# Kernel tuning notes

Hardware: AMD Instinct MI355X
Metric: run time of the kernel (lower is better)

## Reference

```python
import jax, jax.numpy as jnp
import numpy as np

B, N, H, DQK, DV = 2, 2048, 16, 128, 128
E = H * DV
CHUNK = 64


def setup_inputs() -> dict:
    key = jax.random.key(0)
    ks = jax.random.split(key, 11)
    w = lambda k: jax.random.normal(k, (E, E), jnp.float32) * 0.02
    return {
        "x": jax.random.normal(ks[0], (B, N, E), jnp.float32),
        "prev_state": jnp.zeros((B, H, DQK, DV), jnp.float32),
        "Wq": w(ks[1]), "bq": jnp.zeros((E,), jnp.float32),
        "Wk": w(ks[2]), "bk": jnp.zeros((E,), jnp.float32),
        "Wv": w(ks[3]), "bv": jnp.zeros((E,), jnp.float32),
        "Wg": w(ks[4]), "bg": jnp.zeros((E,), jnp.float32),
        "Wo": w(ks[5]), "bo": jnp.zeros((E,), jnp.float32),
        "start_idx": 0,
    }


def _mul_i(t):
    # multiply interleaved complex pairs by i: (a, b) -> (-b, a)
    t2 = t.reshape(*t.shape[:-1], -1, 2)
    return jnp.stack((-t2[..., 1], t2[..., 0]), axis=-1).reshape(t.shape)


def reference(x, prev_state, Wq, bq, Wk, bk, Wv, bv, Wg, bg, Wo, bo, start_idx):
    b, n, e = x.shape
    h, dqk, dv, c = H, DQK, DV, CHUNK
    q = (x @ Wq.T + bq).reshape(b, n, h, dqk)
    k = (x @ Wk.T + bk).reshape(b, n, h, dqk)
    v = (x @ Wv.T + bv).reshape(b, n, h, dv)

    # xPos-style theta shift (rotary on interleaved pairs), applied along the sequence dim
    lin = jnp.linspace(0.0, 1.0, dqk // 2)
    thetas = jnp.repeat(1.0 / (10000.0 ** lin), 2).astype(x.dtype)  # (dqk,)
    idx = (start_idx + jnp.arange(n)).astype(x.dtype)
    ang = idx[:, None] * thetas[None, :]  # (n, dqk)
    sin = jnp.sin(ang)[None, :, None, :]
    cos = jnp.cos(ang)[None, :, None, :]
    q = q * cos + _mul_i(q) * sin
    k = k * cos + _mul_i(k) * sin
    k = k / jnp.sqrt(jnp.asarray(dqk, x.dtype))

    # per-head decays: 1 - 2^(-5 - h)
    gamma = 1.0 - jnp.exp2(-5.0 - jnp.arange(h, dtype=x.dtype))  # (h,)
    i = jnp.arange(c, dtype=x.dtype)
    mask = i[:, None] >= i[None, :]
    Dmat = jnp.where(mask, gamma[:, None, None] ** jnp.where(mask, i[:, None] - i[None, :], 0.0), 0.0)  # (h,c,c)
    cross_decay = gamma[:, None] ** (i[None, :] + 1.0)   # (h,c)
    kv_decay = gamma[:, None] ** (c - 1.0 - i[None, :])  # (h,c)
    chunk_decay = gamma ** c                              # (h,)

    nc = n // c
    qc = q.reshape(b, nc, c, h, dqk).transpose(1, 0, 3, 2, 4)  # (nc,b,h,c,dqk)
    kc = k.reshape(b, nc, c, h, dqk).transpose(1, 0, 3, 2, 4)
    vc = v.reshape(b, nc, c, h, dv).transpose(1, 0, 3, 2, 4)

    def step(S, qkv):
        qi, ki, vi = qkv  # (b,h,c,d)
        att = jnp.einsum('bhid,bhjd->bhij', qi, ki) * Dmat[None]
        o = jnp.einsum('bhij,bhje->bhie', att, vi)
        o = o + jnp.einsum('bhid,bhde->bhie', qi, S) * cross_decay[None, :, :, None]
        S_new = S * chunk_decay[None, :, None, None] + jnp.einsum('bhjd,bhje->bhde', ki * kv_decay[None, :, :, None], vi)
        return S_new, o

    state, outs = jax.lax.scan(step, prev_state, (qc, kc, vc))
    ret = outs.transpose(1, 0, 3, 2, 4).reshape(b, n, h, dv)

    # GroupNorm(num_groups=h, affine=False): normalize each head over dv
    mu = ret.mean(-1, keepdims=True)
    var = ((ret - mu) ** 2).mean(-1, keepdims=True)
    ret = ((ret - mu) / jnp.sqrt(var + 1e-6)).reshape(b, n, e)

    gate = jax.nn.silu(x @ Wg.T + bg)
    out = (ret * gate) @ Wo.T + bo
    return out, state
```

## Files before the change

### kernel.cpp

```cpp
#include <hip/hip_runtime.h>
#include <hip/hip_bf16.h>
#include <stdint.h>

#define B_   2
#define N_   2048
#define H_   16
#define DQK_ 128
#define DV_  128
#define E_   2048
#define CH_  64
#define NC_  32
#define M_   (B_*N_)
#define QKVG_LD 8192

using bf16x8 = __attribute__((ext_vector_type(8))) __bf16;
using f32x4  = __attribute__((ext_vector_type(4))) float;
typedef __hip_bfloat16 bf16_t;

#define ROT_C 0.21091607f
#define KS_   0.08838834764831843f

__device__ __forceinline__ void gload_lds16(const void* g, void* l) {
  __builtin_amdgcn_global_load_lds(
      (const __attribute__((address_space(1))) void*)(uintptr_t)g,
      (__attribute__((address_space(3))) void*)(uint32_t)(uintptr_t)l,
      16, 0, 0);
}

__device__ __forceinline__ float head_log2g(int h) {
  return (float)(log2(1.0 - exp2((double)(-5 - h))));
}

__device__ __forceinline__ float bfu2f(unsigned short u) {
  unsigned int t = (unsigned int)u << 16; float f;
  __builtin_memcpy(&f, &t, 4); return f;
}
__device__ __forceinline__ unsigned short f2bfu(float f) {
  bf16_t b = __float2bfloat16(f);
  unsigned short u; __builtin_memcpy(&u, &b, 2); return u;
}

__device__ __forceinline__ void rot8(const bf16x8& v, float pos, int jp0,
                                     float scale, float* out) {
#pragma unroll
  for (int p = 0; p < 4; p++) {
    float theta = exp2f(-ROT_C * (float)(jp0 + p));
    float ang = pos * theta, s, c;
    sincosf(ang, &s, &c);
    float a = (float)v[2*p], b = (float)v[2*p+1];
    out[2*p]   = (a*c - b*s) * scale;
    out[2*p+1] = (b*c + a*s) * scale;
  }
}

__global__ __launch_bounds__(256)
void cvt_all_kernel(const float* __restrict__ x,
                    const float* __restrict__ Wq, const float* __restrict__ Wk,
                    const float* __restrict__ Wv, const float* __restrict__ Wg,
                    const float* __restrict__ Wo,
                    const float* __restrict__ bq, const float* __restrict__ bk,
                    const float* __restrict__ bv, const float* __restrict__ bg,
                    bf16_t* __restrict__ xb, bf16_t* __restrict__ wcat,
                    bf16_t* __restrict__ wob, float* __restrict__ bcat) {
  const int NX = 2097152, NW = 1048576;
  int g = blockIdx.x * 256 + threadIdx.x;
  const float* s; bf16_t* d; int si, di;
  if (g < NX) { s = x; si = g; d = xb; di = g; }
  else if (g < NX + 4*NW) {
    int t = g - NX; int r = t / NW; si = t - r*NW;
    s = (r==0) ? Wq : (r==1) ? Wk : (r==2) ? Wv : Wg; d = wcat; di = t;
  } else if (g < NX + 5*NW) {
    si = g - NX - 4*NW; s = Wo; d = wob; di = si;
  } else {
    int j = g - (NX + 5*NW);
    int which = j >> 9, i = j & 511;
    const float* bs = (which==0) ? bq : (which==1) ? bk : (which==2) ? bv : bg;
    ((float4*)bcat)[which*512 + i] = ((const float4*)bs)[i];
    return;
  }
  float4 v = ((const float4*)s)[si];
  ushort4 p;
  p.x = f2bfu(v.x); p.y = f2bfu(v.y); p.z = f2bfu(v.z); p.w = f2bfu(v.w);
  ((ushort4*)d)[di] = p;
}

template<bool OUT_BF16, int NSUB>
__global__ __launch_bounds__(512, 2)
void gemm8_kernel(const bf16_t* __restrict__ A, const bf16_t* __restrict__ Bw,
                  const float* __restrict__ bias, void* __restrict__ Cout,
                  int K, int ldc, int tilesN) {
  extern __shared__ char smem[];
  const int nwg = gridDim.x;
  const int bid = blockIdx.x;
  const int cpx = nwg >> 3;
  const int swz = (bid & 7) * cpx + (bid >> 3);
  const int tn = swz % tilesN, tm = swz / tilesN;
  const int rowT0 = tm * 256, colT0 = tn * (64 * NSUB);
  const int tid = threadIdx.x, wave = tid >> 6, lane = tid & 63;
  const int wr = wave >> 2, wc = wave & 3;
  const int l16 = lane & 15, lhi = lane >> 4;
  const int NKT = K >> 6;

  const int sw = ((tid & 7) * 16) ^ (((tid >> 3) & 7) << 4);
  const size_t aOff = (size_t)(rowT0 + (tid >> 3)) * K + (sw >> 1);
  const size_t bOff = (size_t)(colT0 + (tid >> 3)) * K + (sw >> 1);
  const uint32_t wl = wave * 1024;

  auto stage = [&](int h) {
    const int ktp = h >> 2, r = h & 3, buf = ktp & 1;
    const int k0 = ktp << 6;
    if (r < 2) {
      const uint32_t base = 65536u + buf * (8192u*NSUB) + r * (4096u*NSUB) + wl;
#pragma unroll
      for (int L = 0; L < NSUB/2; L++)
        gload_lds16(Bw + bOff + (size_t)(r * (NSUB*32) + L * 64) * K + k0,
                    smem + base + L * 8192);
    } else {
      const int half = r - 2;
      const uint32_t base = buf * 32768u + half * 16384u + wl;
#pragma unroll
      for (int L = 0; L < 2; L++)
        gload_lds16(A + aOff + (size_t)(half * 128 + L * 64) * K + k0,
                    smem + base + L * 8192);
    }
  };

  for (int h = 0; h < 6; h++) stage(h);
  if constexpr (NSUB == 4) asm volatile("s_waitcnt vmcnt(4)" ::: "memory");
  else                     asm volatile("s_waitcnt vmcnt(2)" ::: "memory");
  __builtin_amdgcn_s_barrier();
  asm volatile("" ::: "memory");
  __builtin_amdgcn_sched_barrier(0);

  f32x4 acc[8][NSUB] = {};
  bf16x8 bfr[NSUB][2], bnx[2][2];

#pragma unroll
  for (int n = 0; n < 2; n++) {
    const int r = wc * (16*NSUB) + n * 16 + l16;
#pragma unroll
    for (int ks = 0; ks < 2; ks++) {
      const int cb = ks * 64 + lhi * 16;
      bnx[n][ks] = *(const bf16x8*)(smem + 65536u + r * 128 + (cb ^ ((r & 7) << 4)));
    }
  }

  for (int kt = 0; kt < NKT; kt++) {
    const int cur = kt & 1;
    const uint32_t aB = cur * 32768u;
    const uint32_t bB = 65536u + cur * (8192u*NSUB);
#pragma unroll
    for (int p = 0; p < 4; p++) {
      if (p == 0) {
#pragma unroll
        for (int n = 0; n < 2; n++)
#pragma unroll
          for (int ks = 0; ks < 2; ks++) bfr[n][ks] = bnx[n][ks];
        if constexpr (NSUB == 4) {
#pragma unroll
          for (int n = 2; n < 4; n++) {
            const int r = wc * (16*NSUB) + n * 16 + l16;
#pragma unroll
            for (int ks = 0; ks < 2; ks++) {
              const int cb = ks * 64 + lhi * 16;
              bfr[n][ks] = *(const bf16x8*)(smem + bB + r * 128 + (cb ^ ((r & 7) << 4)));
            }
          }
        }
      }
      bf16x8 afr[2][2];
#pragma unroll
      for (int mm = 0; mm < 2; mm++) {
        const int r = wr * 128 + p * 32 + mm * 16 + l16;
#pragma unroll
        for (int ks = 0; ks < 2; ks++) {
          const int cb = ks * 64 + lhi * 16;
          afr[mm][ks] = *(const bf16x8*)(smem + aB + r * 128 + (cb ^ ((r & 7) << 4)));
        }
      }
      const int h = 4 * kt + p + 6;
      if (h < 4 * NKT) stage(h);
      __builtin_amdgcn_s_barrier();
      asm volatile("s_waitcnt lgkmcnt(0)" ::: "memory");
      __builtin_amdgcn_sched_barrier(0);
      __builtin_amdgcn_s_setprio(1);
#pragma unroll
      for (int mm = 0; mm < 2; mm++)
#pragma unroll
        for (int n = 0; n < NSUB; n++)
#pragma unroll
          for (int ks = 0; ks < 2; ks++)
            acc[2 * p + mm][n] = __builtin_amdgcn_mfma_f32_16x16x32_bf16(
                afr[mm][ks], bfr[n][ks], acc[2 * p + mm][n], 0, 0, 0);
      __builtin_amdgcn_s_setprio(0);
      if (p == 2) {
        if constexpr (NSUB == 4) asm volatile("s_waitcnt vmcnt(6)" ::: "memory");
        else                     asm volatile("s_waitcnt vmcnt(5)" ::: "memory");
      }
      if (p == 3) {
        if (kt < NKT - 2) {
          if constexpr (NSUB == 4) asm volatile("s_waitcnt vmcnt(4)" ::: "memory");
          else                     asm volatile("s_waitcnt vmcnt(2)" ::: "memory");
        } else if (kt == NKT - 2) {
          asm volatile("s_waitcnt vmcnt(0)" ::: "memory");
        }
        if (kt + 1 < NKT) {
          const uint32_t bN = 65536u + ((kt + 1) & 1) * (8192u*NSUB);
#pragma unroll
          for (int n = 0; n < 2; n++) {
            const int r = wc * (16*NSUB) + n * 16 + l16;
#pragma unroll
            for (int ks = 0; ks < 2; ks++) {
              const int cb = ks * 64 + lhi * 16;
              bnx[n][ks] = *(const bf16x8*)(smem + bN + r * 128 + (cb ^ ((r & 7) << 4)));
            }
          }
        }
      }
      __builtin_amdgcn_s_barrier();
      asm volatile("" ::: "memory");
      __builtin_amdgcn_sched_barrier(0);
    }
  }

#pragma unroll
  for (int m = 0; m < 8; m++) {
    const int rbase = rowT0 + wr * 128 + m * 16 + lhi * 4;
#pragma unroll
    for (int n = 0; n < NSUB; n++) {
      const int col = colT0 + wc * (16*NSUB) + n * 16 + l16;
      const float bv = bias[col];
#pragma unroll
      for (int j = 0; j < 4; j++) {
        float v = acc[m][n][j] + bv;
        if (OUT_BF16) ((bf16_t*)Cout)[(size_t)(rbase + j) * ldc + col] = __float2bfloat16(v);
        else          ((float*)Cout)[(size_t)(rbase + j) * ldc + col] = v;
      }
    }
  }
}

__global__ __launch_bounds__(256)
void chunk_kvt_kernel(const bf16_t* __restrict__ kb, const bf16_t* __restrict__ vb,
                      const int* __restrict__ startp, bf16_t* __restrict__ kvt) {
  __shared__ alignas(16) char lds[32768];
  char* vts = lds;
  char* kts = lds + 16384;

  const int tid = threadIdx.x, wave = tid >> 6, lane = tid & 63;
  const int l16 = lane & 15, lhi = lane >> 4;
  const int blk = blockIdx.x;
  const int bh = blk >> 5, ch = blk & 31;
  const int h = bh & (H_ - 1);
  const float log2g = head_log2g(h);
  const int n0 = ch * 64;
  const int start = startp[0];

  const size_t bhbase = (size_t)(bh >> 4) * N_ * QKVG_LD + (size_t)h * 128;

#pragma unroll
  for (int it = 0; it < 4; it++) {
    int j = it*16 + (tid >> 4);
    int e0 = (tid & 15) * 8;
    bf16x8 vv = *(const bf16x8*)(vb + bhbase + (size_t)(n0 + j)*QKVG_LD + e0);
    bf16x8 kk = *(const bf16x8*)(kb + bhbase + (size_t)(n0 + j)*QKVG_LD + e0);
    float kr[8];
    rot8(kk, (float)(start + n0 + j), (tid & 15) * 4, KS_, kr);
    float kvd = exp2f((float)(63 - j) * log2g);
#pragma unroll
    for (int m = 0; m < 8; m++) {
      int e = e0 + m;
      *(__bf16*)(vts + e*128 + ((j*2) ^ ((e&7)<<4))) = vv[m];
      *(__bf16*)(kts + e*128 + ((j*2) ^ ((e&7)<<4))) = (__bf16)(kr[m] * kvd);
    }
  }
  __syncthreads();

  f32x4 acc[2][8] = {};
#pragma unroll
  for (int kk2 = 0; kk2 < 2; kk2++) {
#pragma unroll
    for (int et = 0; et < 2; et++) {
      int e = (2*wave + et)*16 + l16;
      bf16x8 vf = *(const bf16x8*)(vts + e*128 + (((kk2*32 + lhi*8)*2) ^ ((e&7)<<4)));
#pragma unroll
      for (int dt = 0; dt < 8; dt++) {
        int d = dt*16 + l16;
        bf16x8 kf = *(const bf16x8*)(kts + d*128 + (((kk2*32 + lhi*8)*2) ^ ((d&7)<<4)));
        acc[et][dt] = __builtin_amdgcn_mfma_f32_16x16x32_bf16(vf, kf, acc[et][dt], 0, 0, 0);
      }
    }
  }

  const size_t obase = (size_t)blk * 16384;
#pragma unroll
  for (int et = 0; et < 2; et++)
#pragma unroll
    for (int dt = 0; dt < 8; dt++)
#pragma unroll
      for (int j = 0; j < 4; j++) {
        int e = (2*wave + et)*16 + lhi*4 + j;
        int d = dt*16 + l16;
        kvt[obase + e*128 + d] = __float2bfloat16(acc[et][dt][j]);
      }
}

__global__ __launch_bounds__(256)
void state_scan_kernel(const bf16_t* __restrict__ kvt, const float* __restrict__ prev,
                       bf16_t* __restrict__ sbft, float* __restrict__ out_state) {
  int p = blockIdx.x * 256 + threadIdx.x;
  int bh = p >> 14;
  int ed = p & 16383;
  int e = ed >> 7, d = ed & 127;
  int h = bh & (H_ - 1);
  const float cdecay = exp2f(64.0f * head_log2g(h));

  float S = prev[(size_t)bh*16384 + d*128 + e];
  size_t boff = (size_t)bh * (NC_*16384) + ed;
  for (int ch = 0; ch < NC_; ch++) {
    sbft[boff] = __float2bfloat16(S);
    S = S * cdecay + __bfloat162float(kvt[boff]);
    boff += 16384;
  }
  out_state[(size_t)bh*16384 + d*128 + e] = S;
}

__global__ __launch_bounds__(256)
void chunk_out_kernel(const bf16_t* __restrict__ qb, const bf16_t* __restrict__ kb,
                      const bf16_t* __restrict__ vb, const bf16_t* __restrict__ gb,
                      const bf16_t* __restrict__ sbft, const int* __restrict__ startp,
                      bf16_t* __restrict__ gated) {
  __shared__ alignas(16) char lds[32768];
  char* vts = lds;
  char* ats = lds + 16384;
  float* o_lds = (float*)lds;

  const int tid = threadIdx.x, wave = tid >> 6, lane = tid & 63;
  const int l16 = lane & 15, lhi = lane >> 4;
  const int blk = blockIdx.x;
  const int bh = blk >> 5, ch = blk & 31;
  const int h = bh & (H_ - 1);
  const int b = bh >> 4;
  const float log2g = head_log2g(h);
  const int n0 = ch * 64;
  const int start = startp[0];

  const size_t bhbase = (size_t)b * N_ * QKVG_LD + (size_t)h * 128;
  const bf16_t* Srow = sbft + (size_t)blk * 16384;

#pragma unroll
  for (int it = 0; it < 4; it++) {
    int j = it*16 + (tid >> 4);
    int e0 = (tid & 15) * 8;
    bf16x8 vv = *(const bf16x8*)(vb + bhbase + (size_t)(n0 + j)*QKVG_LD + e0);
#pragma unroll
    for (int m = 0; m < 8; m++) {
      int e = e0 + m;
      *(__bf16*)(vts + e*128 + ((j*2) ^ ((e&7)<<4))) = vv[m];
    }
  }

  const float pos_q = (float)(start + n0 + wave*16 + l16);
  bf16x8 qf[4];
#pragma unroll
  for (int dk = 0; dk < 4; dk++) {
    bf16x8 qv = *(const bf16x8*)(qb + bhbase + (size_t)(n0 + wave*16 + l16)*QKVG_LD + dk*32 + lhi*8);
    float qr[8];
    rot8(qv, pos_q, dk*16 + lhi*4, 1.0f, qr);
#pragma unroll
    for (int m = 0; m < 8; m++) qf[dk][m] = (__bf16)qr[m];
  }

  f32x4 aacc[4] = {};
#pragma unroll
  for (int jt = 0; jt < 4; jt++) {
    const float pos_k = (float)(start + n0 + jt*16 + l16);
#pragma unroll
    for (int dk = 0; dk < 4; dk++) {
      bf16x8 kv = *(const bf16x8*)(kb + bhbase + (size_t)(n0 + jt*16 + l16)*QKVG_LD + dk*32 + lhi*8);
      float kr[8];
      rot8(kv, pos_k, dk*16 + lhi*4, KS_, kr);
      bf16x8 kf;
#pragma unroll
      for (int m = 0; m < 8; m++) kf[m] = (__bf16)kr[m];
      aacc[jt] = __builtin_amdgcn_mfma_f32_16x16x32_bf16(qf[dk], kf, aacc[jt], 0, 0, 0);
    }
  }
#pragma unroll
  for (int jt = 0; jt < 4; jt++)
#pragma unroll
    for (int j = 0; j < 4; j++) {
      int i = wave*16 + lhi*4 + j;
      int jc = jt*16 + l16;
      aacc[jt][j] *= (i >= jc) ? exp2f((float)(i - jc) * log2g) : 0.0f;
    }

#pragma unroll
  for (int jt = 0; jt < 4; jt++)
#pragma unroll
    for (int j = 0; j < 4; j++) {
      int i = wave*16 + lhi*4 + j;
      int jc = jt*16 + l16;
      *(__bf16*)(ats + i*128 + ((jc*2) ^ ((i&7)<<4))) = (__bf16)aacc[jt][j];
    }
  __syncthreads();

  f32x4 oacc[8] = {};
#pragma unroll
  for (int et = 0; et < 8; et++) {
#pragma unroll
    for (int dk = 0; dk < 4; dk++) {
      int e = et*16 + l16;
      bf16x8 sf = *(const bf16x8*)(Srow + e*128 + dk*32 + lhi*8);
      oacc[et] = __builtin_amdgcn_mfma_f32_16x16x32_bf16(qf[dk], sf, oacc[et], 0, 0, 0);
    }
  }
#pragma unroll
  for (int j = 0; j < 4; j++) {
    int i = wave*16 + lhi*4 + j;
    float f = exp2f((float)(i + 1) * log2g);
#pragma unroll
    for (int et = 0; et < 8; et++) oacc[et][j] *= f;
  }

#pragma unroll
  for (int kk2 = 0; kk2 < 2; kk2++) {
    int i = wave*16 + l16;
    bf16x8 af = *(const bf16x8*)(ats + i*128 + (((kk2*32 + lhi*8)*2) ^ ((i&7)<<4)));
#pragma unroll
    for (int et = 0; et < 8; et++) {
      int e = et*16 + l16;
      bf16x8 vf = *(const bf16x8*)(vts + e*128 + (((kk2*32 + lhi*8)*2) ^ ((e&7)<<4)));
      oacc[et] = __builtin_amdgcn_mfma_f32_16x16x32_bf16(af, vf, oacc[et], 0, 0, 0);
    }
  }

  __syncthreads();
#pragma unroll
  for (int et = 0; et < 8; et++)
#pragma unroll
    for (int j = 0; j < 4; j++) {
      int i = wave*16 + lhi*4 + j;
      o_lds[i*128 + et*16 + l16] = oacc[et][j];
    }
  __syncthreads();

  for (int rr = 0; rr < 16; rr++) {
    int r = wave*16 + rr;
    float2 xv = *(const float2*)&o_lds[r*128 + lane*2];
    float s = xv.x + xv.y, ss = xv.x*xv.x + xv.y*xv.y;
#pragma unroll
    for (int off = 1; off < 64; off <<= 1) {
      s  += __shfl_xor(s, off);
      ss += __shfl_xor(ss, off);
    }
    float mu  = s * (1.0f/128.0f);
    float inv = rsqrtf(ss * (1.0f/128.0f) - mu*mu + 1e-6f);
    size_t grow = (size_t)b * N_ + (n0 + r);
    unsigned int gg = *(const unsigned int*)(gb + grow*QKVG_LD + h*128 + lane*2);
    float g0 = bfu2f((unsigned short)(gg & 0xffff));
    float g1 = bfu2f((unsigned short)(gg >> 16));
    float r0 = (xv.x - mu) * inv * (g0 / (1.0f + expf(-g0)));
    float r1 = (xv.y - mu) * inv * (g1 / (1.0f + expf(-g1)));
    ushort2 o2; o2.x = f2bfu(r0); o2.y = f2bfu(r1);
    *(ushort2*)(gated + grow*2048 + h*128 + lane*2) = o2;
  }
}

extern "C" void kernel_launch(void* const* d_in, const int* in_sizes, int n_in,
                              void* d_out, int out_size, void* d_ws, size_t ws_size,
                              hipStream_t stream) {
  const float* x    = (const float*)d_in[0];
  const float* prev = (const float*)d_in[1];
  const float* Wq = (const float*)d_in[2];  const float* bq = (const float*)d_in[3];
  const float* Wk = (const float*)d_in[4];  const float* bk = (const float*)d_in[5];
  const float* Wv = (const float*)d_in[6];  const float* bv = (const float*)d_in[7];
  const float* Wg = (const float*)d_in[8];  const float* bg = (const float*)d_in[9];
  const float* Wo = (const float*)d_in[10]; const float* bo = (const float*)d_in[11];
  const int* startp = (const int*)d_in[12];

  float* out = (float*)d_out;
  float* out_state = out + (size_t)B_*N_*E_;

  char* w = (char*)d_ws;
  const size_t XN = (size_t)B_*N_*E_;
  const size_t WN = (size_t)E_*E_;
  bf16_t* xb   = (bf16_t*)w;             w += XN*2;
  bf16_t* qkvg = (bf16_t*)w;             w += (size_t)M_*QKVG_LD*2;
  bf16_t* wob  = (bf16_t*)w;             w += WN*2;
  char*   wcat_region = w;               w += 4*WN*2;
  bf16_t* wcat = (bf16_t*)wcat_region;
  bf16_t* sbft = (bf16_t*)w;             w += (size_t)B_*H_*NC_*16384*2;
  bf16_t* kvt   = (bf16_t*)wcat_region;
  float*  bcat  = (float*)sbft;

  hipFuncSetAttribute(reinterpret_cast<const void*>(gemm8_kernel<true,4>),
                      hipFuncAttributeMaxDynamicSharedMemorySize, 131072);
  hipFuncSetAttribute(reinterpret_cast<const void*>(gemm8_kernel<false,2>),
                      hipFuncAttributeMaxDynamicSharedMemorySize, 98304);

  cvt_all_kernel<<<28680, 256, 0, stream>>>(x, Wq, Wk, Wv, Wg, Wo, bq, bk, bv, bg,
                                            xb, wcat, wob, bcat);

  gemm8_kernel<true,4><<<512, 512, 131072, stream>>>(xb, wcat, bcat, (void*)qkvg,
                                                     E_, QKVG_LD, 32 );

  chunk_kvt_kernel<<<B_*H_*NC_, 256, 0, stream>>>(qkvg + 2048, qkvg + 4096,
                                                  startp, kvt);
  state_scan_kernel<<<(B_*H_*16384)/256, 256, 0, stream>>>(kvt, prev, sbft, out_state);
  chunk_out_kernel<<<B_*H_*NC_, 256, 0, stream>>>(qkvg, qkvg + 2048, qkvg + 4096,
                                                  qkvg + 6144, sbft, startp,
                                                  xb );

  gemm8_kernel<false,2><<<256, 512, 98304, stream>>>(xb, wob, bo, (void*)out,
                                                     E_, E_, 16 );
}
```

Measured before the change: 306.7 us.

## Precompute rotary table, reorder GEMM tile mapping, pair state scan, drop barrier

```diff
diff --git a/kernel.cpp b/kernel.cpp
--- a/kernel.cpp
+++ b/kernel.cpp
@@ -12,13 +12,12 @@
 #define NC_  32
 #define M_   (B_*N_)
 #define QKVG_LD 8192
+#define ROT_C 0.21091607f
+#define KS_   0.08838834764831843f
 
 using bf16x8 = __attribute__((ext_vector_type(8))) __bf16;
 using f32x4  = __attribute__((ext_vector_type(4))) float;
 typedef __hip_bfloat16 bf16_t;
-
-#define ROT_C 0.21091607f
-#define KS_   0.08838834764831843f
 
 __device__ __forceinline__ void gload_lds16(const void* g, void* l) {
   __builtin_amdgcn_global_load_lds(
@@ -38,19 +37,6 @@
 __device__ __forceinline__ unsigned short f2bfu(float f) {
   bf16_t b = __float2bfloat16(f);
   unsigned short u; __builtin_memcpy(&u, &b, 2); return u;
-}
-
-__device__ __forceinline__ void rot8(const bf16x8& v, float pos, int jp0,
-                                     float scale, float* out) {
-#pragma unroll
-  for (int p = 0; p < 4; p++) {
-    float theta = exp2f(-ROT_C * (float)(jp0 + p));
-    float ang = pos * theta, s, c;
-    sincosf(ang, &s, &c);
-    float a = (float)v[2*p], b = (float)v[2*p+1];
-    out[2*p]   = (a*c - b*s) * scale;
-    out[2*p+1] = (b*c + a*s) * scale;
-  }
 }
 
 __global__ __launch_bounds__(256)
@@ -60,8 +46,10 @@
                     const float* __restrict__ Wo,
                     const float* __restrict__ bq, const float* __restrict__ bk,
                     const float* __restrict__ bv, const float* __restrict__ bg,
+                    const int* __restrict__ startp,
                     bf16_t* __restrict__ xb, bf16_t* __restrict__ wcat,
-                    bf16_t* __restrict__ wob, float* __restrict__ bcat) {
+                    bf16_t* __restrict__ wob, float* __restrict__ bcat,
+                    float2* __restrict__ trig) {
   const int NX = 2097152, NW = 1048576;
   int g = blockIdx.x * 256 + threadIdx.x;
   const float* s; bf16_t* d; int si, di;
@@ -71,12 +59,21 @@
     s = (r==0) ? Wq : (r==1) ? Wk : (r==2) ? Wv : Wg; d = wcat; di = t;
   } else if (g < NX + 5*NW) {
     si = g - NX - 4*NW; s = Wo; d = wob; di = si;
-  } else {
+  } else if (g < NX + 5*NW + 2048) {
     int j = g - (NX + 5*NW);
     int which = j >> 9, i = j & 511;
     const float* bs = (which==0) ? bq : (which==1) ? bk : (which==2) ? bv : bg;
     ((float4*)bcat)[which*512 + i] = ((const float4*)bs)[i];
     return;
+  } else {
+    int g2 = g - (NX + 5*NW + 2048);
+    if (g2 < 131072) {
+      int n = g2 >> 6, j = g2 & 63;
+      float ang = (float)(startp[0] + n) * exp2f(-ROT_C * (float)j);
+      float sn, cn; sincosf(ang, &sn, &cn);
+      trig[g2] = make_float2(cn, sn);
+    }
+    return;
   }
   float4 v = ((const float4*)s)[si];
   ushort4 p;
@@ -88,13 +85,13 @@
 __global__ __launch_bounds__(512, 2)
 void gemm8_kernel(const bf16_t* __restrict__ A, const bf16_t* __restrict__ Bw,
                   const float* __restrict__ bias, void* __restrict__ Cout,
-                  int K, int ldc, int tilesN) {
+                  int K, int ldc, int tilesM) {
   extern __shared__ char smem[];
   const int nwg = gridDim.x;
   const int bid = blockIdx.x;
   const int cpx = nwg >> 3;
   const int swz = (bid & 7) * cpx + (bid >> 3);
-  const int tn = swz % tilesN, tm = swz / tilesN;
+  const int tm = swz % tilesM, tn = swz / tilesM;
   const int rowT0 = tm * 256, colT0 = tn * (64 * NSUB);
   const int tid = threadIdx.x, wave = tid >> 6, lane = tid & 63;
   const int wr = wave >> 2, wc = wave & 3;
@@ -180,8 +177,6 @@
       }
       const int h = 4 * kt + p + 6;
       if (h < 4 * NKT) stage(h);
-      __builtin_amdgcn_s_barrier();
-      asm volatile("s_waitcnt lgkmcnt(0)" ::: "memory");
       __builtin_amdgcn_sched_barrier(0);
       __builtin_amdgcn_s_setprio(1);
 #pragma unroll
@@ -242,7 +237,7 @@
 
 __global__ __launch_bounds__(256)
 void chunk_kvt_kernel(const bf16_t* __restrict__ kb, const bf16_t* __restrict__ vb,
-                      const int* __restrict__ startp, bf16_t* __restrict__ kvt) {
+                      const float2* __restrict__ trig, bf16_t* __restrict__ kvt) {
   __shared__ alignas(16) char lds[32768];
   char* vts = lds;
   char* kts = lds + 16384;
@@ -254,7 +249,6 @@
   const int h = bh & (H_ - 1);
   const float log2g = head_log2g(h);
   const int n0 = ch * 64;
-  const int start = startp[0];
 
   const size_t bhbase = (size_t)(bh >> 4) * N_ * QKVG_LD + (size_t)h * 128;
 
@@ -264,9 +258,16 @@
     int e0 = (tid & 15) * 8;
     bf16x8 vv = *(const bf16x8*)(vb + bhbase + (size_t)(n0 + j)*QKVG_LD + e0);
     bf16x8 kk = *(const bf16x8*)(kb + bhbase + (size_t)(n0 + j)*QKVG_LD + e0);
+    const float2* tr = trig + (size_t)(n0 + j)*64 + (tid & 15)*4;
+    float kvd = exp2f((float)(63 - j) * log2g) * KS_;
     float kr[8];
-    rot8(kk, (float)(start + n0 + j), (tid & 15) * 4, KS_, kr);
-    float kvd = exp2f((float)(63 - j) * log2g);
+#pragma unroll
+    for (int p = 0; p < 4; p++) {
+      float2 cs = tr[p];
+      float a = (float)kk[2*p], b2 = (float)kk[2*p+1];
+      kr[2*p]   = (a*cs.x - b2*cs.y);
+      kr[2*p+1] = (b2*cs.x + a*cs.y);
+    }
 #pragma unroll
     for (int m = 0; m < 8; m++) {
       int e = e0 + m;
@@ -308,27 +309,33 @@
 __global__ __launch_bounds__(256)
 void state_scan_kernel(const bf16_t* __restrict__ kvt, const float* __restrict__ prev,
                        bf16_t* __restrict__ sbft, float* __restrict__ out_state) {
-  int p = blockIdx.x * 256 + threadIdx.x;
-  int bh = p >> 14;
-  int ed = p & 16383;
+  int t = blockIdx.x * 256 + threadIdx.x;
+  int bh = t >> 13;
+  int ed = (t & 8191) * 2;
   int e = ed >> 7, d = ed & 127;
   int h = bh & (H_ - 1);
   const float cdecay = exp2f(64.0f * head_log2g(h));
 
-  float S = prev[(size_t)bh*16384 + d*128 + e];
-  size_t boff = (size_t)bh * (NC_*16384) + ed;
+  float S0 = prev[(size_t)bh*16384 + (size_t)d*128 + e];
+  float S1 = prev[(size_t)bh*16384 + (size_t)(d+1)*128 + e];
+  size_t boff = ((size_t)bh * (NC_*16384) + ed) >> 1;
+  const unsigned int* kv2 = (const unsigned int*)kvt;
+  unsigned int* sb2 = (unsigned int*)sbft;
   for (int ch = 0; ch < NC_; ch++) {
-    sbft[boff] = __float2bfloat16(S);
-    S = S * cdecay + __bfloat162float(kvt[boff]);
-    boff += 16384;
-  }
-  out_state[(size_t)bh*16384 + d*128 + e] = S;
+    sb2[boff] = (unsigned int)f2bfu(S0) | ((unsigned int)f2bfu(S1) << 16);
+    unsigned int kv = kv2[boff];
+    S0 = S0 * cdecay + bfu2f((unsigned short)(kv & 0xffff));
+    S1 = S1 * cdecay + bfu2f((unsigned short)(kv >> 16));
+    boff += 8192;
+  }
+  out_state[(size_t)bh*16384 + (size_t)d*128 + e]     = S0;
+  out_state[(size_t)bh*16384 + (size_t)(d+1)*128 + e] = S1;
 }
 
 __global__ __launch_bounds__(256)
 void chunk_out_kernel(const bf16_t* __restrict__ qb, const bf16_t* __restrict__ kb,
                       const bf16_t* __restrict__ vb, const bf16_t* __restrict__ gb,
-                      const bf16_t* __restrict__ sbft, const int* __restrict__ startp,
+                      const bf16_t* __restrict__ sbft, const float2* __restrict__ trig,
                       bf16_t* __restrict__ gated) {
   __shared__ alignas(16) char lds[32768];
   char* vts = lds;
@@ -343,7 +350,6 @@
   const int b = bh >> 4;
   const float log2g = head_log2g(h);
   const int n0 = ch * 64;
-  const int start = startp[0];
 
   const size_t bhbase = (size_t)b * N_ * QKVG_LD + (size_t)h * 128;
   const bf16_t* Srow = sbft + (size_t)blk * 16384;
@@ -360,29 +366,35 @@
     }
   }
 
-  const float pos_q = (float)(start + n0 + wave*16 + l16);
+  const float2* trq = trig + (size_t)(n0 + wave*16 + l16)*64;
   bf16x8 qf[4];
 #pragma unroll
   for (int dk = 0; dk < 4; dk++) {
     bf16x8 qv = *(const bf16x8*)(qb + bhbase + (size_t)(n0 + wave*16 + l16)*QKVG_LD + dk*32 + lhi*8);
-    float qr[8];
-    rot8(qv, pos_q, dk*16 + lhi*4, 1.0f, qr);
-#pragma unroll
-    for (int m = 0; m < 8; m++) qf[dk][m] = (__bf16)qr[m];
+#pragma unroll
+    for (int p = 0; p < 4; p++) {
+      float2 cs = trq[dk*16 + lhi*4 + p];
+      float a = (float)qv[2*p], b2 = (float)qv[2*p+1];
+      qf[dk][2*p]   = (__bf16)(a*cs.x - b2*cs.y);
+      qf[dk][2*p+1] = (__bf16)(b2*cs.x + a*cs.y);
+    }
   }
 
   f32x4 aacc[4] = {};
 #pragma unroll
   for (int jt = 0; jt < 4; jt++) {
-    const float pos_k = (float)(start + n0 + jt*16 + l16);
+    const float2* trk = trig + (size_t)(n0 + jt*16 + l16)*64;
 #pragma unroll
     for (int dk = 0; dk < 4; dk++) {
       bf16x8 kv = *(const bf16x8*)(kb + bhbase + (size_t)(n0 + jt*16 + l16)*QKVG_LD + dk*32 + lhi*8);
-      float kr[8];
-      rot8(kv, pos_k, dk*16 + lhi*4, KS_, kr);
       bf16x8 kf;
 #pragma unroll
-      for (int m = 0; m < 8; m++) kf[m] = (__bf16)kr[m];
+      for (int p = 0; p < 4; p++) {
+        float2 cs = trk[dk*16 + lhi*4 + p];
+        float a = (float)kv[2*p], b2 = (float)kv[2*p+1];
+        kf[2*p]   = (__bf16)((a*cs.x - b2*cs.y) * KS_);
+        kf[2*p+1] = (__bf16)((b2*cs.x + a*cs.y) * KS_);
+      }
       aacc[jt] = __builtin_amdgcn_mfma_f32_16x16x32_bf16(qf[dk], kf, aacc[jt], 0, 0, 0);
     }
   }
@@ -481,6 +493,7 @@
 
   float* out = (float*)d_out;
   float* out_state = out + (size_t)B_*N_*E_;
+  float2* trig = (float2*)out;
 
   char* w = (char*)d_ws;
   const size_t XN = (size_t)B_*N_*E_;
@@ -499,17 +512,17 @@
   hipFuncSetAttribute(reinterpret_cast<const void*>(gemm8_kernel<false,2>),
                       hipFuncAttributeMaxDynamicSharedMemorySize, 98304);
 
-  cvt_all_kernel<<<28680, 256, 0, stream>>>(x, Wq, Wk, Wv, Wg, Wo, bq, bk, bv, bg,
-                                            xb, wcat, wob, bcat);
+  cvt_all_kernel<<<29192, 256, 0, stream>>>(x, Wq, Wk, Wv, Wg, Wo, bq, bk, bv, bg,
+                                            startp, xb, wcat, wob, bcat, trig);
 
   gemm8_kernel<true,4><<<512, 512, 131072, stream>>>(xb, wcat, bcat, (void*)qkvg,
-                                                     E_, QKVG_LD, 32 );
+                                                     E_, QKVG_LD, 16 );
 
   chunk_kvt_kernel<<<B_*H_*NC_, 256, 0, stream>>>(qkvg + 2048, qkvg + 4096,
-                                                  startp, kvt);
-  state_scan_kernel<<<(B_*H_*16384)/256, 256, 0, stream>>>(kvt, prev, sbft, out_state);
+                                                  trig, kvt);
+  state_scan_kernel<<<1024, 256, 0, stream>>>(kvt, prev, sbft, out_state);
   chunk_out_kernel<<<B_*H_*NC_, 256, 0, stream>>>(qkvg, qkvg + 2048, qkvg + 4096,
-                                                  qkvg + 6144, sbft, startp,
+                                                  qkvg + 6144, sbft, trig,
                                                   xb );
 
   gemm8_kernel<false,2><<<256, 512, 98304, stream>>>(xb, wob, bo, (void*)out,
```

Result: faster. 283.4 us (-7.6%).
